# Optimization experiments

Measured on AMD Instinct MI355X. Metric: run time of the kernel, lower is better.

## Reference

```python
import jax, jax.numpy as jnp
import numpy as np

B, C, H, HEADS, WS, TOPK = 16, 112, 64, 4, 4, 128
NWH = H // WS          # 16 windows per side
NWIN = NWH * NWH       # 256 windows
HD = C // HEADS        # 28
SCALE = HD ** -0.5


def _topk_indices():
    # Geometric top-K closest full-res pixels per window center (level 0 of focal attention).
    f = H // NWH  # window stride on full-res grid
    qh = np.arange(NWH) * f + f // 2
    cq = np.stack(np.meshgrid(qh, qh, indexing='ij'), 0).reshape(2, -1)            # (2, NWIN)
    ck = np.stack(np.meshgrid(np.arange(H), np.arange(H), indexing='ij'), 0).reshape(2, -1)  # (2, H*H)
    d = np.sqrt(((cq[:, :, None].astype(np.float32) - ck[:, None, :]) ** 2).sum(0))
    return np.argsort(d, axis=1, kind='stable')[:, :TOPK].astype(np.int32)        # (NWIN, TOPK)


def setup_inputs() -> dict:
    key = jax.random.key(0)
    k1, k2, k3 = jax.random.split(key, 3)
    return {
        'x': jax.random.normal(k1, (B, C, H, H), jnp.float32),
        'Wqkv': jax.random.normal(k2, (3 * C, C), jnp.float32) * 0.02,
        'Wproj': jax.random.normal(k3, (C, C), jnp.float32) * 0.02,
        'bproj': jnp.zeros((C,), jnp.float32),
        'topk_idx': jnp.asarray(_topk_indices()),
    }


def reference(x, Wqkv, Wproj, bproj, topk_idx):
    Bv, Cv, Hv, Wv = x.shape
    nwin = (Hv // WS) * (Wv // WS)
    xt = jnp.transpose(x, (0, 2, 3, 1))                       # (B, H, W, C)
    qkv = jnp.einsum('bhwc,dc->bhwd', xt, Wqkv)               # 1x1 conv == matmul
    q, k, v = jnp.split(qkv, 3, axis=-1)
    # Window-partition queries: (B*nwin, heads, ws^2, hd)
    qw = q.reshape(Bv, Hv // WS, WS, Wv // WS, WS, Cv)
    qw = jnp.transpose(qw, (0, 1, 3, 2, 4, 5)).reshape(Bv * nwin, WS * WS, HEADS, HD)
    qw = jnp.transpose(qw, (0, 2, 1, 3)) * SCALE
    # Gather top-K K/V tokens per window from the full-resolution token list
    kf = k.reshape(Bv, Hv * Wv, HEADS, HD)
    vf = v.reshape(Bv, Hv * Wv, HEADS, HD)
    ksel = kf[:, topk_idx]                                    # (B, nwin, TOPK, heads, hd)
    vsel = vf[:, topk_idx]
    ksel = jnp.transpose(ksel, (0, 1, 3, 2, 4)).reshape(Bv * nwin, HEADS, TOPK, HD)
    vsel = jnp.transpose(vsel, (0, 1, 3, 2, 4)).reshape(Bv * nwin, HEADS, TOPK, HD)
    # Windowed attention over gathered KV
    attn = jax.nn.softmax(jnp.einsum('whqd,whkd->whqk', qw, ksel), axis=-1)
    o = jnp.einsum('whqk,whkd->whqd', attn, vsel)             # (B*nwin, heads, ws^2, hd)
    o = jnp.transpose(o, (0, 2, 1, 3)).reshape(Bv * nwin, WS * WS, Cv)
    # Window reverse -> (B, H, W, C)
    o = o.reshape(Bv, Hv // WS, Wv // WS, WS, WS, Cv)
    o = jnp.transpose(o, (0, 1, 3, 2, 4, 5)).reshape(Bv, Hv, Wv, Cv)
    out = jnp.einsum('bhwc,dc->bhwd', o, Wproj) + bproj
    return jnp.transpose(out, (0, 3, 1, 2))                   # (B, C, H, W)
```

## Files before the change

### kernel.cpp

```cpp
#include <hip/hip_runtime.h>
#include <hip/hip_bf16.h>
#include <cstdint>

#define B_ 16
#define C_ 112
#define HEADS_ 4
#define HD_ 28
#define NWIN_ 256
#define TOPK_ 128
#define D3_ 336
#define SCALE_ 0.18898223650461363f

typedef __attribute__((ext_vector_type(4))) float f32x4;
typedef __attribute__((ext_vector_type(8))) short short8;
typedef unsigned uint4u __attribute__((ext_vector_type(4), aligned(4)));

union Frag { unsigned u[4]; uint4 u4; short8 s; };

__device__ inline unsigned cvtpk(float a, float b) {
    unsigned r;
    asm("v_cvt_pk_bf16_f32 %0, %1, %2" : "=v"(r) : "v"(a), "v"(b));
    return r;
}
__device__ inline float bflo(unsigned u) { return __uint_as_float(u << 16); }
__device__ inline float bfhi(unsigned u) { return __uint_as_float(u & 0xFFFF0000u); }

__global__ __launch_bounds__(256) void wt_kernel(const float* __restrict__ W, const float* __restrict__ Wp,
                                                 uint4* __restrict__ WAq,
                                                 uint4* __restrict__ WAh, uint4* __restrict__ WAl) {
    const int id = blockIdx.x * 256 + threadIdx.x;
    if (id < 5376) {
        const int ks = id / 1344, rem = id % 1344;
        const int tile = rem >> 6, l = rem & 63;
        const int d = tile * 16 + (l & 15);
        const int cb = ks * 32 + (l >> 4) * 8;
        float v[8];
        #pragma unroll
        for (int j = 0; j < 8; ++j) { int c = cb + j; v[j] = (c < C_) ? W[d * C_ + c] : 0.f; }
        uint4 o;
        o.x = cvtpk(v[0], v[1]); o.y = cvtpk(v[2], v[3]);
        o.z = cvtpk(v[4], v[5]); o.w = cvtpk(v[6], v[7]);
        WAq[id] = o;
    } else if (id < 5376 + 1792) {
        const int id2 = id - 5376;
        const int ks = id2 / 448, rem = id2 % 448;
        const int tile = rem >> 6, l = rem & 63;
        const int d = tile * 16 + (l & 15);
        const int cb = ks * 32 + (l >> 4) * 8;
        float v[8];
        #pragma unroll
        for (int j = 0; j < 8; ++j) { int c = cb + j; v[j] = (c < C_) ? Wp[d * C_ + c] : 0.f; }
        unsigned hw_[4], lw_[4];
        #pragma unroll
        for (int p = 0; p < 4; ++p) {
            unsigned hh = cvtpk(v[2 * p], v[2 * p + 1]);
            hw_[p] = hh;
            lw_[p] = cvtpk(v[2 * p] - bflo(hh), v[2 * p + 1] - bfhi(hh));
        }
        WAh[id2] = make_uint4(hw_[0], hw_[1], hw_[2], hw_[3]);
        WAl[id2] = make_uint4(lw_[0], lw_[1], lw_[2], lw_[3]);
    }
}

__global__ __launch_bounds__(256) void qkv_kernel(const float* __restrict__ x,
                                                  const uint4* __restrict__ WAq,
                                                  ushort* __restrict__ qkv) {
    __shared__ unsigned xs[64][132];
    const int hw0 = blockIdx.x << 7;
    const int b = blockIdx.y;
    const int tid = threadIdx.x;
    for (int i = tid; i < 2048; i += 256) {
        const int c2 = i >> 5, j4 = (i & 31) << 2;
        uint4 o = make_uint4(0, 0, 0, 0);
        if (c2 < 56) {
            const float* r0 = x + (((size_t)b * C_ + 2 * c2) << 12) + hw0 + j4;
            float4 a = *(const float4*)r0;
            float4 c = *(const float4*)(r0 + 4096);
            o.x = cvtpk(a.x, c.x); o.y = cvtpk(a.y, c.y);
            o.z = cvtpk(a.z, c.z); o.w = cvtpk(a.w, c.w);
        }
        *(uint4*)&xs[c2][j4] = o;
    }
    __syncthreads();
    const int wv = tid >> 6, l = tid & 63, lq = l & 15, g = l >> 4;
    const int hwl = wv << 5;
    Frag bf[4][2];
    #pragma unroll
    for (int ks = 0; ks < 4; ++ks)
        #pragma unroll
        for (int n = 0; n < 2; ++n) {
            const int col = hwl + (n << 4) + lq;
            const int r0 = (ks << 4) + (g << 2);
            bf[ks][n].u[0] = xs[r0][col]; bf[ks][n].u[1] = xs[r0 + 1][col];
            bf[ks][n].u[2] = xs[r0 + 2][col]; bf[ks][n].u[3] = xs[r0 + 3][col];
        }
    const size_t hwbase = ((size_t)b << 12) + hw0;
    #pragma unroll
    for (int dblk = 0; dblk < 3; ++dblk) {
        f32x4 acc[7][2] = {};
        #pragma unroll
        for (int ks = 0; ks < 4; ++ks) {
            const uint4* wp = WAq + ((ks * 21 + dblk * 7) << 6) + l;
            #pragma unroll
            for (int m = 0; m < 7; ++m) {
                Frag af; af.u4 = wp[m << 6];
                acc[m][0] = __builtin_amdgcn_mfma_f32_16x16x32_bf16(af.s, bf[ks][0].s, acc[m][0], 0, 0, 0);
                acc[m][1] = __builtin_amdgcn_mfma_f32_16x16x32_bf16(af.s, bf[ks][1].s, acc[m][1], 0, 0, 0);
            }
        }
        #pragma unroll
        for (int m = 0; m < 7; ++m) {
            const int d0 = dblk * 112 + (m << 4) + (g << 2);
            #pragma unroll
            for (int n = 0; n < 2; ++n) {
                const int hw = hwl + (n << 4) + lq;
                uint2 o2;
                o2.x = cvtpk(acc[m][n][0], acc[m][n][1]);
                o2.y = cvtpk(acc[m][n][2], acc[m][n][3]);
                *(uint2*)(qkv + (hwbase + hw) * D3_ + d0) = o2;
            }
        }
    }
}

__global__ __launch_bounds__(256) void attn_kernel(const ushort* __restrict__ qkv,
                                                   const int* __restrict__ topk,
                                                   const uint4* __restrict__ WAh,
                                                   const uint4* __restrict__ WAl,
                                                   const float* __restrict__ bp,
                                                   float* __restrict__ out) {
    __shared__ int idxs[TOPK_];
    __shared__ __align__(16) unsigned vsT[4][32][68];
    __shared__ __align__(16) unsigned plds[4][16][68];
    const int bid = blockIdx.x;
    const int xcd = bid & 7, j = bid >> 3;
    const int b = j >> 5;
    const int w = (xcd << 5) | (j & 31);
    const int wy = w >> 4, wx = w & 15;
    const int tid = threadIdx.x;
    const int wv = tid >> 6, l = tid & 63, lq = l & 15, g = l >> 4;
    if (tid < TOPK_) idxs[tid] = topk[w * TOPK_ + tid];
    __syncthreads();
    const int h = wv;
    const size_t bbase = (size_t)(b << 12);
    const int hwq = ((wy * 4 + (lq >> 2)) << 6) + (wx << 2) + (lq & 3);
    Frag qf;
    {
        uint4u t = *(const uint4u*)(qkv + (bbase + hwq) * D3_ + h * HD_ + (g << 3));
        qf.u[0] = t[0]; qf.u[1] = t[1];
        qf.u[2] = (g == 3) ? 0u : t[2];
        qf.u[3] = (g == 3) ? 0u : t[3];
    }
    Frag kf[8];
    #pragma unroll
    for (int m = 0; m < 8; ++m) {
        const int kr = idxs[(m << 4) + lq];
        uint4u t = *(const uint4u*)(qkv + (bbase + kr) * D3_ + C_ + h * HD_ + (g << 3));
        kf[m].u[0] = t[0]; kf[m].u[1] = t[1]; kf[m].u[2] = t[2]; kf[m].u[3] = t[3];
    }
    Frag wah[2][4], wal[2][4];
    #pragma unroll
    for (int mi = 0; mi < 2; ++mi) {
        const int m = (wv << 1) + mi;
        #pragma unroll
        for (int ks = 0; ks < 4; ++ks) {
            if (m < 7) {
                wah[mi][ks].u4 = WAh[((ks * 7 + m) << 6) + l];
                wal[mi][ks].u4 = WAl[((ks * 7 + m) << 6) + l];
            } else {
                wah[mi][ks].u4 = make_uint4(0, 0, 0, 0);
                wal[mi][ks].u4 = make_uint4(0, 0, 0, 0);
            }
        }
    }
    {
        const ushort* v0 = qkv + (bbase + idxs[2 * l]) * D3_ + 2 * C_ + h * HD_;
        const ushort* v1 = qkv + (bbase + idxs[2 * l + 1]) * D3_ + 2 * C_ + h * HD_;
        unsigned w0[14], w1[14];
        { uint4u a = *(const uint4u*)v0;        w0[0]=a[0]; w0[1]=a[1]; w0[2]=a[2]; w0[3]=a[3]; }
        { uint4u a = *(const uint4u*)(v0 + 8);  w0[4]=a[0]; w0[5]=a[1]; w0[6]=a[2]; w0[7]=a[3]; }
        { uint4u a = *(const uint4u*)(v0 + 16); w0[8]=a[0]; w0[9]=a[1]; w0[10]=a[2]; w0[11]=a[3]; }
        { uint2 a = *(const uint2*)(v0 + 24);   w0[12]=a.x; w0[13]=a.y; }
        { uint4u a = *(const uint4u*)v1;        w1[0]=a[0]; w1[1]=a[1]; w1[2]=a[2]; w1[3]=a[3]; }
        { uint4u a = *(const uint4u*)(v1 + 8);  w1[4]=a[0]; w1[5]=a[1]; w1[6]=a[2]; w1[7]=a[3]; }
        { uint4u a = *(const uint4u*)(v1 + 16); w1[8]=a[0]; w1[9]=a[1]; w1[10]=a[2]; w1[11]=a[3]; }
        { uint2 a = *(const uint2*)(v1 + 24);   w1[12]=a.x; w1[13]=a.y; }
        #pragma unroll
        for (int jj = 0; jj < 14; ++jj) {
            vsT[wv][2 * jj][l]     = __builtin_amdgcn_perm(w1[jj], w0[jj], 0x05040100);
            vsT[wv][2 * jj + 1][l] = __builtin_amdgcn_perm(w1[jj], w0[jj], 0x07060302);
        }
    }
    f32x4 sacc[8];
    #pragma unroll
    for (int m = 0; m < 8; ++m) {
        f32x4 z = {0.f, 0.f, 0.f, 0.f};
        sacc[m] = __builtin_amdgcn_mfma_f32_16x16x32_bf16(kf[m].s, qf.s, z, 0, 0, 0);
    }
    float mx = -1e30f;
    #pragma unroll
    for (int m = 0; m < 8; ++m)
        #pragma unroll
        for (int r = 0; r < 4; ++r) { sacc[m][r] *= SCALE_; mx = fmaxf(mx, sacc[m][r]); }
    mx = fmaxf(mx, __shfl_xor(mx, 16, 64));
    mx = fmaxf(mx, __shfl_xor(mx, 32, 64));
    float sum = 0.f;
    #pragma unroll
    for (int m = 0; m < 8; ++m)
        #pragma unroll
        for (int r = 0; r < 4; ++r) { float e = __expf(sacc[m][r] - mx); sacc[m][r] = e; sum += e; }
    sum += __shfl_xor(sum, 16, 64);
    sum += __shfl_xor(sum, 32, 64);
    const float inv = 1.f / sum;
    #pragma unroll
    for (int m = 0; m < 8; ++m) {
        unsigned u0 = cvtpk(sacc[m][0] * inv, sacc[m][1] * inv);
        unsigned u1 = cvtpk(sacc[m][2] * inv, sacc[m][3] * inv);
        *(uint2*)&plds[wv][lq][(m << 3) + (g << 1)] = make_uint2(u0, u1);
    }
    f32x4 oacc[2] = {};
    #pragma unroll
    for (int ks = 0; ks < 4; ++ks) {
        Frag pb;
        pb.u4 = *(const uint4*)&plds[wv][lq][(g << 2) + (ks << 4)];
        #pragma unroll
        for (int m = 0; m < 2; ++m) {
            Frag va;
            va.u4 = *(const uint4*)&vsT[wv][lq + (m << 4)][(g << 2) + (ks << 4)];
            oacc[m] = __builtin_amdgcn_mfma_f32_16x16x32_bf16(va.s, pb.s, oacc[m], 0, 0, 0);
        }
    }
    __syncthreads();
    float* os = (float*)&plds[0][0][0];
    for (int i = 1904 + tid; i < 2176; i += 256) os[i] = 0.f;
    #pragma unroll
    for (int m = 0; m < 2; ++m) {
        const int d0 = (g << 2) + (m << 4);
        if (d0 < HD_) {
            #pragma unroll
            for (int r = 0; r < 4; ++r)
                os[(h * HD_ + d0 + r) * 17 + lq] = oacc[m][r];
        }
    }
    __syncthreads();
    f32x4 pacc[2] = {};
    #pragma unroll
    for (int ks = 0; ks < 4; ++ks) {
        const int cb = (g << 3) + (ks << 5);
        float v[8];
        #pragma unroll
        for (int jj = 0; jj < 8; ++jj) v[jj] = os[(cb + jj) * 17 + lq];
        Frag bh, bl;
        #pragma unroll
        for (int p = 0; p < 4; ++p) {
            unsigned hh = cvtpk(v[2 * p], v[2 * p + 1]);
            bh.u[p] = hh;
            bl.u[p] = cvtpk(v[2 * p] - bflo(hh), v[2 * p + 1] - bfhi(hh));
        }
        #pragma unroll
        for (int mi = 0; mi < 2; ++mi) {
            pacc[mi] = __builtin_amdgcn_mfma_f32_16x16x32_bf16(wah[mi][ks].s, bh.s, pacc[mi], 0, 0, 0);
            pacc[mi] = __builtin_amdgcn_mfma_f32_16x16x32_bf16(wah[mi][ks].s, bl.s, pacc[mi], 0, 0, 0);
            pacc[mi] = __builtin_amdgcn_mfma_f32_16x16x32_bf16(wal[mi][ks].s, bh.s, pacc[mi], 0, 0, 0);
        }
    }
    #pragma unroll
    for (int mi = 0; mi < 2; ++mi) {
        const int m = (wv << 1) + mi;
        if (m < 7) {
            const int d0 = (m << 4) + (g << 2);
            const float4 bias = *(const float4*)(bp + d0);
            out[(((size_t)(b * C_ + d0 + 0)) << 12) + hwq] = pacc[mi][0] + bias.x;
            out[(((size_t)(b * C_ + d0 + 1)) << 12) + hwq] = pacc[mi][1] + bias.y;
            out[(((size_t)(b * C_ + d0 + 2)) << 12) + hwq] = pacc[mi][2] + bias.z;
            out[(((size_t)(b * C_ + d0 + 3)) << 12) + hwq] = pacc[mi][3] + bias.w;
        }
    }
}

extern "C" void kernel_launch(void* const* d_in, const int* in_sizes, int n_in,
                              void* d_out, int out_size, void* d_ws, size_t ws_size,
                              hipStream_t stream) {
    const float* x     = (const float*)d_in[0];
    const float* Wqkv  = (const float*)d_in[1];
    const float* Wproj = (const float*)d_in[2];
    const float* bproj = (const float*)d_in[3];
    const int*   topk  = (const int*)d_in[4];
    float* out = (float*)d_out;
    char* ws = (char*)d_ws;
    ushort* qkv = (ushort*)ws;
    uint4*  WAq = (uint4*)(ws + 44040192);
    uint4*  WAh = (uint4*)(ws + 44040192 + 86016);
    uint4*  WAl = (uint4*)(ws + 44040192 + 86016 + 28672);
    wt_kernel<<<28, 256, 0, stream>>>(Wqkv, Wproj, WAq, WAh, WAl);
    qkv_kernel<<<dim3(32, 16), 256, 0, stream>>>(x, WAq, qkv);
    attn_kernel<<<dim3(NWIN_ * B_), 256, 0, stream>>>(qkv, topk, WAh, WAl, bproj, out);
}
```

Measured before the change: 160.7 us.

## Split QKV projection across output blocks; drop LDS index staging in attention

The QKV kernel now launches one block per (hw tile, output third, batch), so the grid grows from 512 to 1536 blocks. Each block loads and converts the same x tile that previously served all three output thirds, trading redundant x reads for more parallelism and less register pressure. The attention kernel reads top-k indices straight from global memory instead of staging them in LDS behind a barrier. It also issues the V gathers early and defers their LDS transpose until after softmax, with launch bounds hinting three blocks per CU, to overlap gather latency with compute.

Measured after the change: 146.5 us. -8.8%, faster.

```diff
diff --git a/kernel.cpp b/kernel.cpp
--- a/kernel.cpp
+++ b/kernel.cpp
@@ -67,7 +67,8 @@
                                                   ushort* __restrict__ qkv) {
     __shared__ unsigned xs[64][132];
     const int hw0 = blockIdx.x << 7;
-    const int b = blockIdx.y;
+    const int dblk = blockIdx.y;
+    const int b = blockIdx.z;
     const int tid = threadIdx.x;
     for (int i = tid; i < 2048; i += 256) {
         const int c2 = i >> 5, j4 = (i & 31) << 2;
@@ -84,52 +85,46 @@
     __syncthreads();
     const int wv = tid >> 6, l = tid & 63, lq = l & 15, g = l >> 4;
     const int hwl = wv << 5;
-    Frag bf[4][2];
-    #pragma unroll
-    for (int ks = 0; ks < 4; ++ks)
+    f32x4 acc[7][2] = {};
+    #pragma unroll
+    for (int ks = 0; ks < 4; ++ks) {
+        Frag bf[2];
         #pragma unroll
         for (int n = 0; n < 2; ++n) {
             const int col = hwl + (n << 4) + lq;
             const int r0 = (ks << 4) + (g << 2);
-            bf[ks][n].u[0] = xs[r0][col]; bf[ks][n].u[1] = xs[r0 + 1][col];
-            bf[ks][n].u[2] = xs[r0 + 2][col]; bf[ks][n].u[3] = xs[r0 + 3][col];
-        }
+            bf[n].u[0] = xs[r0][col]; bf[n].u[1] = xs[r0 + 1][col];
+            bf[n].u[2] = xs[r0 + 2][col]; bf[n].u[3] = xs[r0 + 3][col];
+        }
+        const uint4* wp = WAq + ((ks * 21 + dblk * 7) << 6) + l;
+        #pragma unroll
+        for (int m = 0; m < 7; ++m) {
+            Frag af; af.u4 = wp[m << 6];
+            acc[m][0] = __builtin_amdgcn_mfma_f32_16x16x32_bf16(af.s, bf[0].s, acc[m][0], 0, 0, 0);
+            acc[m][1] = __builtin_amdgcn_mfma_f32_16x16x32_bf16(af.s, bf[1].s, acc[m][1], 0, 0, 0);
+        }
+    }
     const size_t hwbase = ((size_t)b << 12) + hw0;
     #pragma unroll
-    for (int dblk = 0; dblk < 3; ++dblk) {
-        f32x4 acc[7][2] = {};
-        #pragma unroll
-        for (int ks = 0; ks < 4; ++ks) {
-            const uint4* wp = WAq + ((ks * 21 + dblk * 7) << 6) + l;
-            #pragma unroll
-            for (int m = 0; m < 7; ++m) {
-                Frag af; af.u4 = wp[m << 6];
-                acc[m][0] = __builtin_amdgcn_mfma_f32_16x16x32_bf16(af.s, bf[ks][0].s, acc[m][0], 0, 0, 0);
-                acc[m][1] = __builtin_amdgcn_mfma_f32_16x16x32_bf16(af.s, bf[ks][1].s, acc[m][1], 0, 0, 0);
-            }
-        }
-        #pragma unroll
-        for (int m = 0; m < 7; ++m) {
-            const int d0 = dblk * 112 + (m << 4) + (g << 2);
-            #pragma unroll
-            for (int n = 0; n < 2; ++n) {
-                const int hw = hwl + (n << 4) + lq;
-                uint2 o2;
-                o2.x = cvtpk(acc[m][n][0], acc[m][n][1]);
-                o2.y = cvtpk(acc[m][n][2], acc[m][n][3]);
-                *(uint2*)(qkv + (hwbase + hw) * D3_ + d0) = o2;
-            }
-        }
-    }
-}
-
-__global__ __launch_bounds__(256) void attn_kernel(const ushort* __restrict__ qkv,
-                                                   const int* __restrict__ topk,
-                                                   const uint4* __restrict__ WAh,
-                                                   const uint4* __restrict__ WAl,
-                                                   const float* __restrict__ bp,
-                                                   float* __restrict__ out) {
-    __shared__ int idxs[TOPK_];
+    for (int m = 0; m < 7; ++m) {
+        const int d0 = dblk * 112 + (m << 4) + (g << 2);
+        #pragma unroll
+        for (int n = 0; n < 2; ++n) {
+            const int hw = hwl + (n << 4) + lq;
+            uint2 o2;
+            o2.x = cvtpk(acc[m][n][0], acc[m][n][1]);
+            o2.y = cvtpk(acc[m][n][2], acc[m][n][3]);
+            *(uint2*)(qkv + (hwbase + hw) * D3_ + d0) = o2;
+        }
+    }
+}
+
+__global__ __launch_bounds__(256, 3) void attn_kernel(const ushort* __restrict__ qkv,
+                                                      const int* __restrict__ topk,
+                                                      const uint4* __restrict__ WAh,
+                                                      const uint4* __restrict__ WAl,
+                                                      const float* __restrict__ bp,
+                                                      float* __restrict__ out) {
     __shared__ __align__(16) unsigned vsT[4][32][68];
     __shared__ __align__(16) unsigned plds[4][16][68];
     const int bid = blockIdx.x;
@@ -139,11 +134,10 @@
     const int wy = w >> 4, wx = w & 15;
     const int tid = threadIdx.x;
     const int wv = tid >> 6, l = tid & 63, lq = l & 15, g = l >> 4;
-    if (tid < TOPK_) idxs[tid] = topk[w * TOPK_ + tid];
-    __syncthreads();
     const int h = wv;
     const size_t bbase = (size_t)(b << 12);
     const int hwq = ((wy * 4 + (lq >> 2)) << 6) + (wx << 2) + (lq & 3);
+    const int* tkw = topk + (w << 7);
     Frag qf;
     {
         uint4u t = *(const uint4u*)(qkv + (bbase + hwq) * D3_ + h * HD_ + (g << 3));
@@ -154,9 +148,23 @@
     Frag kf[8];
     #pragma unroll
     for (int m = 0; m < 8; ++m) {
-        const int kr = idxs[(m << 4) + lq];
+        const int kr = tkw[(m << 4) + lq];
         uint4u t = *(const uint4u*)(qkv + (bbase + kr) * D3_ + C_ + h * HD_ + (g << 3));
         kf[m].u[0] = t[0]; kf[m].u[1] = t[1]; kf[m].u[2] = t[2]; kf[m].u[3] = t[3];
+    }
+    unsigned w0[14], w1[14];
+    {
+        const int2 vidx = *(const int2*)(tkw + 2 * l);
+        const ushort* v0 = qkv + (bbase + vidx.x) * D3_ + 2 * C_ + h * HD_;
+        const ushort* v1 = qkv + (bbase + vidx.y) * D3_ + 2 * C_ + h * HD_;
+        { uint4u a = *(const uint4u*)v0;        w0[0]=a[0]; w0[1]=a[1]; w0[2]=a[2]; w0[3]=a[3]; }
+        { uint4u a = *(const uint4u*)(v0 + 8);  w0[4]=a[0]; w0[5]=a[1]; w0[6]=a[2]; w0[7]=a[3]; }
+        { uint4u a = *(const uint4u*)(v0 + 16); w0[8]=a[0]; w0[9]=a[1]; w0[10]=a[2]; w0[11]=a[3]; }
+        { uint2 a = *(const uint2*)(v0 + 24);   w0[12]=a.x; w0[13]=a.y; }
+        { uint4u a = *(const uint4u*)v1;        w1[0]=a[0]; w1[1]=a[1]; w1[2]=a[2]; w1[3]=a[3]; }
+        { uint4u a = *(const uint4u*)(v1 + 8);  w1[4]=a[0]; w1[5]=a[1]; w1[6]=a[2]; w1[7]=a[3]; }
+        { uint4u a = *(const uint4u*)(v1 + 16); w1[8]=a[0]; w1[9]=a[1]; w1[10]=a[2]; w1[11]=a[3]; }
+        { uint2 a = *(const uint2*)(v1 + 24);   w1[12]=a.x; w1[13]=a.y; }
     }
     Frag wah[2][4], wal[2][4];
     #pragma unroll
@@ -173,24 +181,6 @@
             }
         }
     }
-    {
-        const ushort* v0 = qkv + (bbase + idxs[2 * l]) * D3_ + 2 * C_ + h * HD_;
-        const ushort* v1 = qkv + (bbase + idxs[2 * l + 1]) * D3_ + 2 * C_ + h * HD_;
-        unsigned w0[14], w1[14];
-        { uint4u a = *(const uint4u*)v0;        w0[0]=a[0]; w0[1]=a[1]; w0[2]=a[2]; w0[3]=a[3]; }
-        { uint4u a = *(const uint4u*)(v0 + 8);  w0[4]=a[0]; w0[5]=a[1]; w0[6]=a[2]; w0[7]=a[3]; }
-        { uint4u a = *(const uint4u*)(v0 + 16); w0[8]=a[0]; w0[9]=a[1]; w0[10]=a[2]; w0[11]=a[3]; }
-        { uint2 a = *(const uint2*)(v0 + 24);   w0[12]=a.x; w0[13]=a.y; }
-        { uint4u a = *(const uint4u*)v1;        w1[0]=a[0]; w1[1]=a[1]; w1[2]=a[2]; w1[3]=a[3]; }
-        { uint4u a = *(const uint4u*)(v1 + 8);  w1[4]=a[0]; w1[5]=a[1]; w1[6]=a[2]; w1[7]=a[3]; }
-        { uint4u a = *(const uint4u*)(v1 + 16); w1[8]=a[0]; w1[9]=a[1]; w1[10]=a[2]; w1[11]=a[3]; }
-        { uint2 a = *(const uint2*)(v1 + 24);   w1[12]=a.x; w1[13]=a.y; }
-        #pragma unroll
-        for (int jj = 0; jj < 14; ++jj) {
-            vsT[wv][2 * jj][l]     = __builtin_amdgcn_perm(w1[jj], w0[jj], 0x05040100);
-            vsT[wv][2 * jj + 1][l] = __builtin_amdgcn_perm(w1[jj], w0[jj], 0x07060302);
-        }
-    }
     f32x4 sacc[8];
     #pragma unroll
     for (int m = 0; m < 8; ++m) {
@@ -217,6 +207,11 @@
         unsigned u0 = cvtpk(sacc[m][0] * inv, sacc[m][1] * inv);
         unsigned u1 = cvtpk(sacc[m][2] * inv, sacc[m][3] * inv);
         *(uint2*)&plds[wv][lq][(m << 3) + (g << 1)] = make_uint2(u0, u1);
+    }
+    #pragma unroll
+    for (int jj = 0; jj < 14; ++jj) {
+        vsT[wv][2 * jj][l]     = __builtin_amdgcn_perm(w1[jj], w0[jj], 0x05040100);
+        vsT[wv][2 * jj + 1][l] = __builtin_amdgcn_perm(w1[jj], w0[jj], 0x07060302);
     }
     f32x4 oacc[2] = {};
     #pragma unroll
@@ -293,6 +288,6 @@
     uint4*  WAh = (uint4*)(ws + 44040192 + 86016);
     uint4*  WAl = (uint4*)(ws + 44040192 + 86016 + 28672);
     wt_kernel<<<28, 256, 0, stream>>>(Wqkv, Wproj, WAq, WAh, WAl);
-    qkv_kernel<<<dim3(32, 16), 256, 0, stream>>>(x, WAq, qkv);
+    qkv_kernel<<<dim3(32, 3, 16), 256, 0, stream>>>(x, WAq, qkv);
     attn_kernel<<<dim3(NWIN_ * B_), 256, 0, stream>>>(qkv, topk, WAh, WAl, bproj, out);
 }
```
